# Kernel optimization log

Measured on AMD Instinct MI355X. Metric: run time of the kernel, lower is better.

The kernel has to match this reference:

```python
import jax, jax.numpy as jnp
import numpy as np

B, L, D = 2, 2048, 2048
HQ, HKV = 32, 8
HD = D // HQ  # 64
ROPE_BASE = 10000.0
ROPE_SCALE = 1.0


def setup_inputs() -> dict:
    key = jax.random.key(0)
    ks = jax.random.split(key, 5)
    s = 0.02
    return {
        "x": jax.random.normal(ks[0], (B, L, D), dtype=jnp.float32),
        "pos_ids": jnp.arange(L, dtype=jnp.int64) if jax.config.jax_enable_x64 else jnp.arange(L, dtype=jnp.int32),
        "wq": jax.random.normal(ks[1], (D, D), dtype=jnp.float32) * s,
        "wk": jax.random.normal(ks[2], (HKV * HD, D), dtype=jnp.float32) * s,
        "wv": jax.random.normal(ks[3], (HKV * HD, D), dtype=jnp.float32) * s,
        "wo": jax.random.normal(ks[4], (D, D), dtype=jnp.float32) * s,
    }


def _rope_cos_sin(pos_ids, rot_dim, dtype):
    half = rot_dim // 2
    idx = jnp.arange(half, dtype=jnp.float32)
    inv_freq = (1.0 / (ROPE_BASE ** (idx / half))) * ROPE_SCALE  # [half]
    freqs = pos_ids.astype(dtype)[:, None] * inv_freq.astype(dtype)[None, :]  # [L, half]
    return jnp.cos(freqs), jnp.sin(freqs)


def _apply_rotary(x, cos, sin):
    # x: [B, L, H, Hd]; interleaved pair rotation on full head dim
    b, l, h, hd = x.shape
    xp = x.reshape(b, l, h, hd // 2, 2)
    x1, x2 = xp[..., 0], xp[..., 1]
    c = cos.reshape(1, l, 1, hd // 2)
    s = sin.reshape(1, l, 1, hd // 2)
    y1 = x1 * c - x2 * s
    y2 = x1 * s + x2 * c
    return jnp.stack([y1, y2], axis=-1).reshape(b, l, h, hd)


def reference(x, pos_ids, wq, wk, wv, wo):
    b, l, d = x.shape
    q = (x @ wq.T).reshape(b, l, HQ, HD)
    k = (x @ wk.T).reshape(b, l, HKV, HD)
    v = (x @ wv.T).reshape(b, l, HKV, HD)

    cos, sin = _rope_cos_sin(pos_ids, HD, x.dtype)
    q = _apply_rotary(q, cos, sin)
    k = _apply_rotary(k, cos, sin)

    group = HQ // HKV  # GQA: each kv head serves `group` consecutive q heads
    k = jnp.repeat(k, group, axis=2)  # [b, l, HQ, HD]
    v = jnp.repeat(v, group, axis=2)

    scale = 1.0 / jnp.sqrt(jnp.asarray(HD, dtype=x.dtype))
    scores = jnp.einsum("bqhd,bkhd->bhqk", q, k) * scale  # [b, HQ, l, l]
    causal = jnp.tril(jnp.ones((l, l), dtype=bool))
    neg = jnp.asarray(jnp.finfo(x.dtype).min, dtype=x.dtype)
    scores = jnp.where(causal[None, None], scores, neg)
    attn = jax.nn.softmax(scores, axis=-1)
    out = jnp.einsum("bhqk,bkhd->bqhd", attn, v).reshape(b, l, d)
    return out @ wo.T
```

## Files before the change

### kernel.cpp

```cpp
#include <hip/hip_runtime.h>
#include <stdint.h>

typedef unsigned short u16;
typedef unsigned int   u32;
typedef __bf16 bf16_t;
typedef bf16_t bf16x8 __attribute__((ext_vector_type(8)));
typedef u16    u16x8  __attribute__((ext_vector_type(8)));
typedef float  f32x4  __attribute__((ext_vector_type(4)));
typedef float  f32x16 __attribute__((ext_vector_type(16)));

#define NB   2
#define NL   2048
#define ND   2048
#define NHQ  32
#define NHKV 8
#define NHD  64
#define NQKV 3072
#define QSCALE 0.18033688011112042f
#define SM_SHIFT 24.0f

__device__ __forceinline__ u16 f2bf(float x){
  union{float f;u32 u;} v; v.f = x;
  u32 r = v.u + 0x7FFFu + ((v.u >> 16) & 1u);
  return (u16)(r >> 16);
}
__device__ __forceinline__ float bf2f(u16 b){
  union{u32 u;float f;} v; v.u = ((u32)b) << 16; return v.f;
}

__device__ __forceinline__ float exp2_hw(float x){
#if __has_builtin(__builtin_amdgcn_exp2f)
  return __builtin_amdgcn_exp2f(x);
#else
  float r; asm("v_exp_f32 %0, %1" : "=v"(r) : "v"(x)); return r;
#endif
}

__device__ __forceinline__ void gload_lds16(const void* g, void* l){
  auto gp = reinterpret_cast<__attribute__((address_space(1))) u16*>(
      (uintptr_t)g);
  auto lp = reinterpret_cast<__attribute__((address_space(3))) u16*>(
      (uintptr_t)l);
  __builtin_amdgcn_global_load_lds(gp, lp, 16, 0, 0);
}

__device__ __forceinline__ f32x4 mfma16(bf16x8 a, bf16x8 b, f32x4 c){
  return __builtin_amdgcn_mfma_f32_16x16x32_bf16(a, b, c, 0, 0, 0);
}
__device__ __forceinline__ f32x16 mfma32(bf16x8 a, bf16x8 b, f32x16 c){
  return __builtin_amdgcn_mfma_f32_32x32x16_bf16(a, b, c, 0, 0, 0);
}
__device__ __forceinline__ u32 cvtpk(float lo, float hi){
  u32 w;
  asm("v_cvt_pk_bf16_f32 %0, %1, %2" : "=v"(w) : "v"(lo), "v"(hi));
  return w;
}

#define CV_S1 2097152
#define CV_S2 3145728
#define CV_S3 3407872
#define CV_S4 3670016
#define CV_S5 4718592
#define CV_TOT (CV_S5 + 65536)

__global__ void k_prep(const float* __restrict__ x,  const float* __restrict__ wq,
                       const float* __restrict__ wk, const float* __restrict__ wv,
                       const float* __restrict__ wo, const int* __restrict__ pos,
                       u16* __restrict__ xb, u16* __restrict__ wqkvb, u16* __restrict__ wob,
                       float* __restrict__ cosT, float* __restrict__ sinT){
  int i = blockIdx.x * 256 + threadIdx.x;
  if (i < CV_S5){
    const float4* src; ushort4* dst; int off;
    if (i < CV_S1)      { src = (const float4*)x;  dst = (ushort4*)xb;    off = i; }
    else if (i < CV_S2) { src = (const float4*)wq; dst = (ushort4*)wqkvb; off = i - CV_S1; }
    else if (i < CV_S3) { src = (const float4*)wk; dst = (ushort4*)wqkvb + 1048576; off = i - CV_S2; }
    else if (i < CV_S4) { src = (const float4*)wv; dst = (ushort4*)wqkvb + 1310720; off = i - CV_S3; }
    else                { src = (const float4*)wo; dst = (ushort4*)wob;   off = i - CV_S4; }
    float4 f = src[off];
    ushort4 o;
    o.x = f2bf(f.x); o.y = f2bf(f.y); o.z = f2bf(f.z); o.w = f2bf(f.w);
    dst[off] = o;
  } else {
    int idx = i - CV_S5;
    int l = idx >> 5, k = idx & 31;
    float p = (float)pos[l];
    float inv = __expf(-((float)k * (1.0f/32.0f)) * 9.210340371976184f);
    float fr = p * inv;
    cosT[idx] = cosf(fr);
    sinT[idx] = sinf(fr);
  }
}

template<int BM, int BN, int WRITE_F32>
__global__ __launch_bounds__(512) void k_gemm8(const u16* __restrict__ A,
                                               const u16* __restrict__ Bm,
                                               void* __restrict__ Cp,
                                               int M, int N, int K){
  constexpr int LA_N = BM/64;
  constexpr int LB_N = BN/64;
  constexpr int LN   = LA_N + LB_N;
  constexpr int MR   = BM/32;
  constexpr int MH   = MR/2;
  constexpr int NF   = BN/64;
  __shared__ u16 LA[2][BM*64];
  __shared__ u16 LB[2][BN*64];
  const int tid = threadIdx.x;
  const int lane = tid & 63, w = tid >> 6;
  const int wr = w >> 2, wc = w & 3;
  const int lr = lane & 15, lg = lane >> 4;
  const int tn = blockIdx.x * BN, tm = blockIdx.y * BM;
  const size_t Kb = (size_t)K * 2;
  const char* Ab = (const char*)A;
  const char* Bb = (const char*)Bm;

  u32 soff[LN]; int ldoff[LN];
#pragma unroll
  for (int l = 0; l < LN; ++l){
    int o = ((l < LA_N) ? l : (l - LA_N))*8192 + tid*16;
    int s = o ^ (((o>>7)&7)<<4);
    int row = s >> 7, col = s & 127;
    int trow = (l < LA_N) ? (tm + row) : (tn + row);
    soff[l]  = (u32)((size_t)trow * Kb + col);
    ldoff[l] = o;
  }
  const int c0 = ( lg      ^ (lr & 7)) << 4;
  const int c1 = ((4 + lg) ^ (lr & 7)) << 4;
  const int arow = (wr*(BM/2) + lr) * 128;
  const int brow = (wc*(BN/4) + lr) * 128;

  f32x4 acc[MR][NF] = {};
  const int NT = K >> 6;

#pragma unroll
  for (int l = 0; l < LN; ++l){
    char* base = (l < LA_N) ? (char*)LA[0] : (char*)LB[0];
    const char* gb = (l < LA_N) ? Ab : Bb;
    gload_lds16(gb + soff[l], base + ldoff[l]);
  }
  asm volatile("s_waitcnt vmcnt(0)" ::: "memory");
  __builtin_amdgcn_s_barrier();

#pragma unroll 1
  for (int kt = 0; kt < NT; ++kt){
    const int cur = kt & 1;
    const char* la = (const char*)LA[cur] + arow;
    const char* lb = (const char*)LB[cur] + brow;
    char* nA = (char*)LA[cur^1];
    char* nB = (char*)LB[cur^1];
    const u32 koff = (u32)(kt+1) * 128;
    const bool pre = (kt + 1 < NT);

    bf16x8 bf[NF][2], af[MH][2];

#define PH2(p)                                                                \
    {                                                                         \
      if ((p) == 0){                                                          \
        _Pragma("unroll")                                                     \
        for (int n = 0; n < NF; ++n){                                         \
          bf[n][0] = *(const bf16x8*)(lb + n*2048 + c0);                      \
          bf[n][1] = *(const bf16x8*)(lb + n*2048 + c1);                      \
        }                                                                     \
      }                                                                       \
      _Pragma("unroll")                                                       \
      for (int q = 0; q < MH; ++q){                                           \
        af[q][0] = *(const bf16x8*)(la + (MH*(p)+q)*2048 + c0);               \
        af[q][1] = *(const bf16x8*)(la + (MH*(p)+q)*2048 + c1);               \
      }                                                                       \
      if ((p) == 0 && pre){                                                   \
        _Pragma("unroll")                                                     \
        for (int l = 0; l < LN; ++l){                                         \
          char* nb_ = (l < LA_N) ? nA : nB;                                   \
          const char* gb_ = (l < LA_N) ? Ab : Bb;                             \
          gload_lds16(gb_ + soff[l] + koff, nb_ + ldoff[l]);                  \
        }                                                                     \
      }                                                                       \
      __builtin_amdgcn_s_barrier();                                           \
      asm volatile("s_waitcnt lgkmcnt(0)" ::: "memory");                      \
      __builtin_amdgcn_sched_barrier(0);                                      \
      __builtin_amdgcn_s_setprio(1);                                          \
      _Pragma("unroll")                                                       \
      for (int q = 0; q < MH; ++q){                                           \
        _Pragma("unroll")                                                     \
        for (int n = 0; n < NF; ++n){                                         \
          acc[MH*(p)+q][n] = mfma16(af[q][0], bf[n][0], acc[MH*(p)+q][n]);    \
          acc[MH*(p)+q][n] = mfma16(af[q][1], bf[n][1], acc[MH*(p)+q][n]);    \
        }                                                                     \
      }                                                                       \
      __builtin_amdgcn_s_setprio(0);                                          \
    }

    PH2(0)
    __builtin_amdgcn_s_barrier();
    PH2(1)
    asm volatile("s_waitcnt vmcnt(0)" ::: "memory");
    __builtin_amdgcn_s_barrier();
#undef PH2
  }

  const int rb = tm + wr*(BM/2) + lg*4;
  const int cb = tn + wc*(BN/4) + lr;
#pragma unroll
  for (int m = 0; m < MR; ++m){
#pragma unroll
    for (int n = 0; n < NF; ++n){
#pragma unroll
      for (int r = 0; r < 4; ++r){
        size_t off = (size_t)(rb + m*16 + r) * N + (cb + n*16);
        if (WRITE_F32) ((float*)Cp)[off] = acc[m][n][r];
        else           ((u16*)Cp)[off]   = f2bf(acc[m][n][r]);
      }
    }
  }
}

__global__ void k_rope_scatter(const u16* __restrict__ qkv, const float* __restrict__ cosT,
                               const float* __restrict__ sinT,
                               u16* __restrict__ Q, u16* __restrict__ Ko, u16* __restrict__ V){
  const int row = blockIdx.x;
  const int b = row >> 11, l = row & 2047;
  const int t = threadIdx.x;
#pragma unroll
  for (int it = 0; it < 6; ++it){
    int pp = t + it*256;
    u32 xin = *reinterpret_cast<const u32*>(&qkv[(size_t)row*NQKV + pp*2]);
    float x1 = bf2f((u16)(xin & 0xFFFFu));
    float x2 = bf2f((u16)(xin >> 16));
    if (pp < 1280){
      int i = pp & 31;
      float c = cosT[l*32 + i], s = sinT[l*32 + i];
      float y1 = x1*c - x2*s;
      float y2 = x1*s + x2*c;
      if (pp < 1024){
        int hh = pp >> 5, d = (pp & 31)*2;
        u32 o = (u32)f2bf(y1*QSCALE) | ((u32)f2bf(y2*QSCALE) << 16);
        *reinterpret_cast<u32*>(&Q[(((size_t)(b*NHQ + hh))*NL + l)*NHD + d]) = o;
      } else {
        int idx = pp - 1024, kvh = idx >> 5, d = (idx & 31)*2;
        u32 o = (u32)f2bf(y1) | ((u32)f2bf(y2) << 16);
        *reinterpret_cast<u32*>(&Ko[(((size_t)(b*NHKV + kvh))*NL + l)*NHD + d]) = o;
      }
    } else {
      int idx = pp - 1280, kvh = idx >> 5, d = (idx & 31)*2;
      *reinterpret_cast<u32*>(&V[(((size_t)(b*NHKV + kvh))*NL + l)*NHD + d]) = xin;
    }
  }
}

__global__ __launch_bounds__(256) void k_transpose(const u16* __restrict__ V, u16* __restrict__ VT){
  __shared__ u16 T[64*72];
  const int bid = blockIdx.x;
  const int slice = bid >> 5, tile = bid & 31;
  const u16* src = V  + (size_t)slice*NL*NHD + (size_t)tile*64*NHD;
  u16*       dst = VT + (size_t)slice*NHD*NL + (size_t)tile*64;
  const int t = threadIdx.x;
  {
    int r = t >> 2, c0 = (t & 3)*16;
    const u16x8* s = reinterpret_cast<const u16x8*>(src + (size_t)r*NHD + c0);
    *reinterpret_cast<u16x8*>(&T[r*72 + c0])     = s[0];
    *reinterpret_cast<u16x8*>(&T[r*72 + c0 + 8]) = s[1];
  }
  __syncthreads();
  {
    int d = t >> 2, l0 = (t & 3)*16;
    u16x8 v0, v1;
#pragma unroll
    for (int j = 0; j < 8; ++j) v0[j] = T[(l0+j)*72 + d];
#pragma unroll
    for (int j = 0; j < 8; ++j) v1[j] = T[(l0+8+j)*72 + d];
    u16* dp = dst + (size_t)d*NL + l0;
    *reinterpret_cast<u16x8*>(dp)     = v0;
    *reinterpret_cast<u16x8*>(dp + 8) = v1;
  }
}

__device__ __forceinline__ void stage_kv32(const u16* __restrict__ Kp, const u16* __restrict__ VTp,
                                           int kvb, u16* lk, u16* lv, int w, int lane){
  const char* ks = (const char*)(Kp + (size_t)kvb*NHD);
  const char* vs = (const char*)VTp + (size_t)kvb*2;
  const int o = w*1024 + lane*16;
  const int swk = o ^ (((o>>7)&7)<<4);
  gload_lds16(ks + swk, (char*)lk + w*1024);
  const int row = o >> 6, c = o & 63;
  gload_lds16(vs + (size_t)row*(NL*2) + (c ^ (((row>>1)&3)<<4)), (char*)lv + w*1024);
}
__device__ __forceinline__ bf16x8 ldsK(const u16* base, int row, int colb){
  return *reinterpret_cast<const bf16x8*>((const char*)base + row*128 + (colb ^ ((row&7)<<4)));
}
__device__ __forceinline__ bf16x8 ldsV(const u16* base, int row, int colb){
  return *reinterpret_cast<const bf16x8*>((const char*)base + row*64 + (colb ^ (((row>>1)&3)<<4)));
}

__global__ __launch_bounds__(256) void k_attn7(const u16* __restrict__ Q, const u16* __restrict__ Kg,
                                               const u16* __restrict__ VT, u16* __restrict__ O){
  __shared__ u16 LK[2][2048];
  __shared__ u16 LV[2][2048];
  const int tid = threadIdx.x, lane = tid & 63, w = tid >> 6;
  const int q32 = lane & 31, hi = lane >> 5;
  const int f = blockIdx.x;
  const int round = f >> 8, c = f & 255;
  const int i16 = c >> 4;
  const int qti = round*16 + ((round & 1) ? (15 - i16) : i16);
  const int qt = 63 - qti;
  const int grp = c & 15;
  const int b = grp >> 3, kvh = grp & 7;
  const int h = kvh*4 + w;
  const u16* Qp  = Q  + ((size_t)(b*NHQ  + h  ))*NL*NHD;
  const u16* Kp  = Kg + ((size_t)(b*NHKV + kvh))*NL*NHD;
  const u16* VTp = VT + ((size_t)(b*NHKV + kvh))*NHD*NL;

  const int qrow = qt*32 + q32;
  const int ntw  = qt + 1;

  bf16x8 qf[4];
#pragma unroll
  for (int ks = 0; ks < 4; ++ks)
    qf[ks] = *reinterpret_cast<const bf16x8*>(&Qp[(size_t)qrow*NHD + ks*16 + hi*8]);

  f32x16 o0 = {}, o1 = {};
  float lsum = 0.0f;

  stage_kv32(Kp, VTp, 0, LK[0], LV[0], w, lane);
  __syncthreads();

#pragma unroll 1
  for (int j = 0; j < ntw; ++j){
    const int cur = j & 1;
    const u16* lk = LK[cur];
    const u16* lv = LV[cur];
    if (j + 1 < ntw)
      stage_kv32(Kp, VTp, (j+1) << 5, LK[cur^1], LV[cur^1], w, lane);

    const int kvb = j << 5;
    bf16x8 kf[4];
#pragma unroll
    for (int ks = 0; ks < 4; ++ks)
      kf[ks] = ldsK(lk, q32, ks*32 + hi*16);
    f32x16 s0 = {};
    __builtin_amdgcn_s_setprio(1);
#pragma unroll
    for (int ks = 0; ks < 4; ++ks)
      s0 = mfma32(kf[ks], qf[ks], s0);
    __builtin_amdgcn_s_setprio(0);
    if (j == ntw - 1){
#pragma unroll
      for (int r = 0; r < 16; ++r){
        const int kl = (r&3) + 8*(r>>2) + 4*hi;
        if (kvb + kl > qrow) s0[r] = -1e30f;
      }
    }
#pragma unroll
    for (int r = 0; r < 16; ++r) s0[r] = exp2_hw(s0[r] - SM_SHIFT);
    float u[8];
#pragma unroll
    for (int r = 0; r < 8; ++r)  u[r] = s0[r] + s0[r+8];
#pragma unroll
    for (int r = 0; r < 4; ++r)  u[r] += u[r+4];
    lsum += (u[0]+u[1]) + (u[2]+u[3]);
    u32 wds[8];
#pragma unroll
    for (int i = 0; i < 8; ++i) wds[i] = cvtpk(s0[2*i], s0[2*i+1]);
    bf16x8 pf[2];
#pragma unroll
    for (int fi = 0; fi < 2; ++fi){
      u32 x  = wds[4*fi+0], y  = wds[4*fi+2];
      u32 x2 = wds[4*fi+1], y2 = wds[4*fi+3];
      asm("v_permlane32_swap_b32 %0, %1" : "+v"(x),  "+v"(y));
      asm("v_permlane32_swap_b32 %0, %1" : "+v"(x2), "+v"(y2));
      union { u32 wq[4]; bf16x8 v; } uu;
      uu.wq[0] = x; uu.wq[1] = x2; uu.wq[2] = y; uu.wq[3] = y2;
      pf[fi] = uu.v;
    }
    bf16x8 vf[4];
    vf[0] = ldsV(lv, q32,      hi*16);
    vf[1] = ldsV(lv, q32,      32 + hi*16);
    vf[2] = ldsV(lv, 32 + q32, hi*16);
    vf[3] = ldsV(lv, 32 + q32, 32 + hi*16);
    __builtin_amdgcn_s_setprio(1);
    o0 = mfma32(vf[0], pf[0], o0);
    o0 = mfma32(vf[1], pf[1], o0);
    o1 = mfma32(vf[2], pf[0], o1);
    o1 = mfma32(vf[3], pf[1], o1);
    __builtin_amdgcn_s_setprio(0);
    __syncthreads();
  }

  float lt = lsum + __shfl_xor(lsum, 32);
  const float inv = 1.0f / lt;
  u16* Op = O + ((size_t)(b*NL + qrow))*ND + h*NHD;
#pragma unroll
  for (int md = 0; md < 2; ++md){
#pragma unroll
    for (int q4 = 0; q4 < 4; ++q4){
      ushort4 sv;
      float a0 = (md ? o1[4*q4+0] : o0[4*q4+0]) * inv;
      float a1 = (md ? o1[4*q4+1] : o0[4*q4+1]) * inv;
      float a2 = (md ? o1[4*q4+2] : o0[4*q4+2]) * inv;
      float a3 = (md ? o1[4*q4+3] : o0[4*q4+3]) * inv;
      sv.x = f2bf(a0); sv.y = f2bf(a1); sv.z = f2bf(a2); sv.w = f2bf(a3);
      *reinterpret_cast<ushort4*>(&Op[md*32 + 8*q4 + 4*hi]) = sv;
    }
  }
}

extern "C" void kernel_launch(void* const* d_in, const int* in_sizes, int n_in,
                              void* d_out, int out_size, void* d_ws, size_t ws_size,
                              hipStream_t stream){
  (void)in_sizes; (void)n_in; (void)out_size; (void)ws_size;
  const float* x   = (const float*)d_in[0];
  const int*   pos = (const int*)  d_in[1];
  const float* wq  = (const float*)d_in[2];
  const float* wk  = (const float*)d_in[3];
  const float* wv  = (const float*)d_in[4];
  const float* wo  = (const float*)d_in[5];

  char* ws = (char*)d_ws;
  size_t off = 0;
  auto alloc = [&](size_t bytes) -> void* {
    void* p = ws + off;
    off += (bytes + 255) & ~(size_t)255;
    return p;
  };
  const size_t n_x   = (size_t)NB*NL*ND;
  const size_t n_wq  = (size_t)ND*ND;

  u16* xb    = (u16*)alloc(n_x*2);
  u16* wqkvb = (u16*)alloc((size_t)NQKV*ND*2);
  u16* wob   = (u16*)alloc(n_wq*2);
  u16* qkv   = (u16*)alloc((size_t)NB*NL*NQKV*2);
  u16* Qb    = (u16*)alloc((size_t)NB*NHQ*NL*NHD*2);
  u16* Kb    = (u16*)alloc((size_t)NB*NHKV*NL*NHD*2);
  u16* Vb    = (u16*)alloc((size_t)NB*NHKV*NL*NHD*2);
  u16* VTb   = (u16*)alloc((size_t)NB*NHKV*NHD*NL*2);
  float* cosT= (float*)alloc((size_t)NL*32*4);
  float* sinT= (float*)alloc((size_t)NL*32*4);

  k_prep<<<CV_TOT/256, 256, 0, stream>>>(x, wq, wk, wv, wo, pos, xb, wqkvb, wob, cosT, sinT);

  k_gemm8<256,192,0><<<dim3(NQKV/192, (NB*NL)/256), 512, 0, stream>>>(xb, wqkvb, qkv, NB*NL, NQKV, ND);
  k_rope_scatter<<<NB*NL, 256, 0, stream>>>(qkv, cosT, sinT, Qb, Kb, Vb);
  k_transpose<<<NB*NHKV*(NL/64), 256, 0, stream>>>(Vb, VTb);
  k_attn7<<<1024, 256, 0, stream>>>(Qb, Kb, VTb, xb);
  k_gemm8<128,256,1><<<dim3(ND/256, (NB*NL)/128), 512, 0, stream>>>(xb, wob, d_out, NB*NL, ND, ND);
}
```

Measured before the change: 176.0 us.

## Software-pipeline GEMM LDS fragment loads across k-tiles with partial lgkm waits

Restructures the bf16 GEMM main loop to unroll by two k-tiles with ping-pong register fragments. The next tile's A and B fragments are read from LDS while the current tile's second-half MFMAs run, and partial lgkmcnt waits replace full drains. The goal is to hide LDS read latency behind matrix math and cut barrier stalls. It needs more registers for the double fragment sets and relies on hand-tuned wait counts, which risks spills or ordering bugs.

```diff
diff --git a/kernel.cpp b/kernel.cpp
--- a/kernel.cpp
+++ b/kernel.cpp
@@ -54,6 +54,16 @@
   u32 w;
   asm("v_cvt_pk_bf16_f32 %0, %1, %2" : "=v"(w) : "v"(lo), "v"(hi));
   return w;
+}
+
+template<int N> __device__ __forceinline__ void lgkm_wait(){
+  if      constexpr (N == 0)  asm volatile("s_waitcnt lgkmcnt(0)"  ::: "memory");
+  else if constexpr (N == 4)  asm volatile("s_waitcnt lgkmcnt(4)"  ::: "memory");
+  else if constexpr (N == 8)  asm volatile("s_waitcnt lgkmcnt(8)"  ::: "memory");
+  else if constexpr (N == 12) asm volatile("s_waitcnt lgkmcnt(12)" ::: "memory");
+  else if constexpr (N == 14) asm volatile("s_waitcnt lgkmcnt(14)" ::: "memory");
+  else                        asm volatile("s_waitcnt lgkmcnt(15)" ::: "memory");
+  __builtin_amdgcn_sched_barrier(0);
 }
 
 #define CV_S1 2097152
@@ -92,7 +102,7 @@
 }
 
 template<int BM, int BN, int WRITE_F32>
-__global__ __launch_bounds__(512) void k_gemm8(const u16* __restrict__ A,
+__global__ __launch_bounds__(512) void k_gemm9(const u16* __restrict__ A,
                                                const u16* __restrict__ Bm,
                                                void* __restrict__ Cp,
                                                int M, int N, int K){
@@ -102,8 +112,8 @@
   constexpr int MR   = BM/32;
   constexpr int MH   = MR/2;
   constexpr int NF   = BN/64;
-  __shared__ u16 LA[2][BM*64];
-  __shared__ u16 LB[2][BN*64];
+  __shared__ u16 LAb[2][BM*64];
+  __shared__ u16 LBb[2][BN*64];
   const int tid = threadIdx.x;
   const int lane = tid & 63, w = tid >> 6;
   const int wr = w >> 2, wc = w & 3;
@@ -129,73 +139,93 @@
   const int brow = (wc*(BN/4) + lr) * 128;
 
   f32x4 acc[MR][NF] = {};
+  bf16x8 bfA[NF][2], bfB[NF][2], afA[MH][2], afB[MH][2];
   const int NT = K >> 6;
 
 #pragma unroll
   for (int l = 0; l < LN; ++l){
-    char* base = (l < LA_N) ? (char*)LA[0] : (char*)LB[0];
+    char* base = (l < LA_N) ? (char*)LAb[0] : (char*)LBb[0];
     const char* gb = (l < LA_N) ? Ab : Bb;
     gload_lds16(gb + soff[l], base + ldoff[l]);
   }
   asm volatile("s_waitcnt vmcnt(0)" ::: "memory");
   __builtin_amdgcn_s_barrier();
+#pragma unroll
+  for (int n = 0; n < NF; ++n){
+    bfA[n][0] = *(const bf16x8*)((const char*)LBb[0] + brow + n*2048 + c0);
+    bfA[n][1] = *(const bf16x8*)((const char*)LBb[0] + brow + n*2048 + c1);
+  }
+#pragma unroll
+  for (int q = 0; q < MH; ++q){
+    afA[q][0] = *(const bf16x8*)((const char*)LAb[0] + arow + q*2048 + c0);
+    afA[q][1] = *(const bf16x8*)((const char*)LAb[0] + arow + q*2048 + c1);
+  }
+
+#define TILE(laC, laN, lbN, bfc, bfn, PRE, KOFF)                            \
+    {                                                                       \
+                            \
+      _Pragma("unroll")                                                     \
+      for (int q = 0; q < MH; ++q){                                         \
+        afB[q][0] = *(const bf16x8*)((const char*)(laC) + arow + (MH+q)*2048 + c0); \
+        afB[q][1] = *(const bf16x8*)((const char*)(laC) + arow + (MH+q)*2048 + c1); \
+      }                                                                     \
+      if (PRE){                                                             \
+        _Pragma("unroll")                                                   \
+        for (int l = 0; l < LN; ++l){                                       \
+          char* nb_ = (l < LA_N) ? (char*)(laN) : (char*)(lbN);             \
+          const char* gb_ = (l < LA_N) ? Ab : Bb;                           \
+          gload_lds16(gb_ + soff[l] + (KOFF), nb_ + ldoff[l]);              \
+        }                                                                   \
+      }                                                                     \
+      lgkm_wait<2*MH>();                                                    \
+      __builtin_amdgcn_s_setprio(1);                                        \
+      _Pragma("unroll")                                                     \
+      for (int q = 0; q < MH; ++q){                                         \
+        _Pragma("unroll")                                                   \
+        for (int n = 0; n < NF; ++n){                                       \
+          acc[q][n] = mfma16(afA[q][0], bfc[n][0], acc[q][n]);              \
+          acc[q][n] = mfma16(afA[q][1], bfc[n][1], acc[q][n]);              \
+        }                                                                   \
+      }                                                                     \
+      __builtin_amdgcn_s_setprio(0);                                        \
+      asm volatile("s_waitcnt vmcnt(0)" ::: "memory");                      \
+      __builtin_amdgcn_s_barrier();                                         \
+                        \
+      if (PRE){                                                             \
+        _Pragma("unroll")                                                   \
+        for (int n = 0; n < NF; ++n){                                       \
+          bfn[n][0] = *(const bf16x8*)((const char*)(lbN) + brow + n*2048 + c0); \
+          bfn[n][1] = *(const bf16x8*)((const char*)(lbN) + brow + n*2048 + c1); \
+        }                                                                   \
+        _Pragma("unroll")                                                   \
+        for (int q = 0; q < MH; ++q){                                       \
+          afA[q][0] = *(const bf16x8*)((const char*)(laN) + arow + q*2048 + c0); \
+          afA[q][1] = *(const bf16x8*)((const char*)(laN) + arow + q*2048 + c1); \
+        }                                                                   \
+        lgkm_wait<2*NF + 2*MH>();                                           \
+      } else {                                                              \
+        lgkm_wait<0>();                                                     \
+      }                                                                     \
+      __builtin_amdgcn_s_setprio(1);                                        \
+      _Pragma("unroll")                                                     \
+      for (int q = 0; q < MH; ++q){                                         \
+        _Pragma("unroll")                                                   \
+        for (int n = 0; n < NF; ++n){                                       \
+          acc[MH+q][n] = mfma16(afB[q][0], bfc[n][0], acc[MH+q][n]);        \
+          acc[MH+q][n] = mfma16(afB[q][1], bfc[n][1], acc[MH+q][n]);        \
+        }                                                                   \
+      }                                                                     \
+      __builtin_amdgcn_s_setprio(0);                                        \
+      __builtin_amdgcn_s_barrier();                                         \
+    }
 
 #pragma unroll 1
-  for (int kt = 0; kt < NT; ++kt){
-    const int cur = kt & 1;
-    const char* la = (const char*)LA[cur] + arow;
-    const char* lb = (const char*)LB[cur] + brow;
-    char* nA = (char*)LA[cur^1];
-    char* nB = (char*)LB[cur^1];
-    const u32 koff = (u32)(kt+1) * 128;
-    const bool pre = (kt + 1 < NT);
-
-    bf16x8 bf[NF][2], af[MH][2];
-
-#define PH2(p)                                                                \
-    {                                                                         \
-      if ((p) == 0){                                                          \
-        _Pragma("unroll")                                                     \
-        for (int n = 0; n < NF; ++n){                                         \
-          bf[n][0] = *(const bf16x8*)(lb + n*2048 + c0);                      \
-          bf[n][1] = *(const bf16x8*)(lb + n*2048 + c1);                      \
-        }                                                                     \
-      }                                                                       \
-      _Pragma("unroll")                                                       \
-      for (int q = 0; q < MH; ++q){                                           \
-        af[q][0] = *(const bf16x8*)(la + (MH*(p)+q)*2048 + c0);               \
-        af[q][1] = *(const bf16x8*)(la + (MH*(p)+q)*2048 + c1);               \
-      }                                                                       \
-      if ((p) == 0 && pre){                                                   \
-        _Pragma("unroll")                                                     \
-        for (int l = 0; l < LN; ++l){                                         \
-          char* nb_ = (l < LA_N) ? nA : nB;                                   \
-          const char* gb_ = (l < LA_N) ? Ab : Bb;                             \
-          gload_lds16(gb_ + soff[l] + koff, nb_ + ldoff[l]);                  \
-        }                                                                     \
-      }                                                                       \
-      __builtin_amdgcn_s_barrier();                                           \
-      asm volatile("s_waitcnt lgkmcnt(0)" ::: "memory");                      \
-      __builtin_amdgcn_sched_barrier(0);                                      \
-      __builtin_amdgcn_s_setprio(1);                                          \
-      _Pragma("unroll")                                                       \
-      for (int q = 0; q < MH; ++q){                                           \
-        _Pragma("unroll")                                                     \
-        for (int n = 0; n < NF; ++n){                                         \
-          acc[MH*(p)+q][n] = mfma16(af[q][0], bf[n][0], acc[MH*(p)+q][n]);    \
-          acc[MH*(p)+q][n] = mfma16(af[q][1], bf[n][1], acc[MH*(p)+q][n]);    \
-        }                                                                     \
-      }                                                                       \
-      __builtin_amdgcn_s_setprio(0);                                          \
-    }
-
-    PH2(0)
-    __builtin_amdgcn_s_barrier();
-    PH2(1)
-    asm volatile("s_waitcnt vmcnt(0)" ::: "memory");
-    __builtin_amdgcn_s_barrier();
-#undef PH2
-  }
+  for (int kt = 0; kt < NT; kt += 2){
+    const bool pre1 = (kt + 2 < NT);
+    TILE(LAb[0], LAb[1], LBb[1], bfA, bfB, true, (u32)(kt+1)*128)
+    TILE(LAb[1], LAb[0], LBb[0], bfB, bfA, pre1, (u32)(kt+2)*128)
+  }
+#undef TILE
 
   const int rb = tm + wr*(BM/2) + lg*4;
   const int cb = tn + wc*(BN/4) + lr;
@@ -436,9 +466,9 @@
 
   k_prep<<<CV_TOT/256, 256, 0, stream>>>(x, wq, wk, wv, wo, pos, xb, wqkvb, wob, cosT, sinT);
 
-  k_gemm8<256,192,0><<<dim3(NQKV/192, (NB*NL)/256), 512, 0, stream>>>(xb, wqkvb, qkv, NB*NL, NQKV, ND);
+  k_gemm9<256,192,0><<<dim3(NQKV/192, (NB*NL)/256), 512, 0, stream>>>(xb, wqkvb, qkv, NB*NL, NQKV, ND);
   k_rope_scatter<<<NB*NL, 256, 0, stream>>>(qkv, cosT, sinT, Qb, Kb, Vb);
   k_transpose<<<NB*NHKV*(NL/64), 256, 0, stream>>>(Vb, VTb);
   k_attn7<<<1024, 256, 0, stream>>>(Qb, Kb, VTb, xb);
-  k_gemm8<128,256,1><<<dim3(ND/256, (NB*NL)/128), 512, 0, stream>>>(xb, wob, d_out, NB*NL, ND, ND);
-}
+  k_gemm9<128,256,1><<<dim3(ND/256, (NB*NL)/128), 512, 0, stream>>>(xb, wob, d_out, NB*NL, ND, ND);
+}
```

Result: slower. 179.5 us (+2.0%).
